# Kernel tuning notes

Hardware: AMD Instinct MI355X
Metric: run time of the kernel (lower is better)

## Reference

```python
import jax, jax.numpy as jnp
import numpy as np

N, E, B = 50000, 800000, 64
F_IN, HID, H, L = 128, 128, 4, 4
C = HID // H  # per-head channels = 32
NEG_SLOPE = 0.2  # PyG GATConv default leaky_relu slope


def setup_inputs() -> dict:
    key = jax.random.key(0)
    ks = iter(jax.random.split(key, 32))
    rn = lambda shape, s=0.05: jax.random.normal(next(ks), shape, jnp.float32) * s
    x = jax.random.normal(next(ks), (N, F_IN), jnp.float32)
    edge_index = jax.random.randint(next(ks), (2, E), 0, N, jnp.int32)
    edge_attr = jax.random.uniform(next(ks), (E, 2), dtype=jnp.float32)
    batch = jnp.sort(jax.random.randint(next(ks), (N,), 0, B, jnp.int32))
    return {
        "x": x, "edge_attr": edge_attr,
        "Win": rn((F_IN, HID)), "b_in": jnp.zeros((HID,), jnp.float32),
        "We1": rn((2, 16)), "be1": jnp.zeros((16,), jnp.float32),
        "We2": rn((16, H)), "be2": jnp.zeros((H,), jnp.float32),
        "Wl": rn((L, HID, HID)), "a_src": rn((L, H, C)), "a_dst": rn((L, H, C)),
        "bl": jnp.zeros((L, HID), jnp.float32),
        "ln_g": jnp.ones((L, HID), jnp.float32), "ln_b": jnp.zeros((L, HID), jnp.float32),
        "Wg1": rn((HID, HID // 2)), "bg1": jnp.zeros((HID // 2,), jnp.float32),
        "Wg2": rn((HID // 2, 1)), "bg2": jnp.zeros((1,), jnp.float32),
        "edge_index": edge_index, "batch": batch,
    }


def _layer_norm(x, g, b, eps=1e-5):
    mu = x.mean(-1, keepdims=True)
    var = ((x - mu) ** 2).mean(-1, keepdims=True)
    return (x - mu) * jax.lax.rsqrt(var + eps) * g + b


def _gat_conv(h, src, dst, W, a_s, a_d, bias):
    # PyG GATConv (shared lin for src/dst), add_self_loops already in src/dst.
    xp = (h @ W).reshape(N, H, C)            # [N,H,C]
    as_n = (xp * a_s).sum(-1)                # [N,H]
    ad_n = (xp * a_d).sum(-1)                # [N,H]
    e = jax.nn.leaky_relu(as_n[src] + ad_n[dst], NEG_SLOPE)   # [E+N,H]
    m = jax.ops.segment_max(e, dst, num_segments=N)           # stable softmax per dst
    p = jnp.exp(e - m[dst])
    s = jax.ops.segment_sum(p, dst, num_segments=N)
    alpha = p / (s[dst] + 1e-16)
    out = jax.ops.segment_sum(xp[src] * alpha[..., None], dst, num_segments=N)
    return out.reshape(N, HID) + bias


def reference(x, edge_attr, Win, b_in, We1, be1, We2, be2, Wl, a_src, a_dst, bl,
              ln_g, ln_b, Wg1, bg1, Wg2, bg2, edge_index, batch):
    h = x @ Win + b_in                                   # input_proj
    # edge bias MLP -> per-edge scalar -> scatter_add crit_signal (no self loops)
    edge_bias = jax.nn.relu(edge_attr @ We1 + be1) @ We2 + be2   # [E,H]
    edge_scalar = edge_bias.mean(axis=1)                         # [E]
    crit = jnp.zeros((N,), h.dtype).at[edge_index[1]].add(edge_scalar)[:, None]
    # self loops for GATConv
    loop = jnp.arange(N, dtype=edge_index.dtype)
    src = jnp.concatenate([edge_index[0], loop])
    dst = jnp.concatenate([edge_index[1], loop])
    for i in range(L):  # fixed small layer count
        h_new = _gat_conv(h, src, dst, Wl[i], a_src[i], a_dst[i], bl[i])
        h_new = _layer_norm(h_new, ln_g[i], ln_b[i])
        h_new = h_new + crit                             # broadcast [N,1]
        h = h_new + h                                    # residual (shapes match); dropout=eval noop
    # GlobalAttention pooling: softmax(gate) over each graph, weighted sum
    gate = jnp.tanh(h @ Wg1 + bg1) @ Wg2 + bg2           # [N,1]
    gmax = jax.ops.segment_max(gate, batch, num_segments=B)
    gp = jnp.exp(gate - gmax[batch])
    gs = jax.ops.segment_sum(gp, batch, num_segments=B)
    gate_sm = gp / (gs[batch] + 1e-16)
    return jax.ops.segment_sum(gate_sm * h, batch, num_segments=B)   # [B,HID]
```

## Files before the change

### kernel.cpp

```cpp
#include <hip/hip_runtime.h>
#include <math.h>

#define N_NODES 50000
#define N_EDGES 800000
#define N_B     64

typedef __attribute__((ext_vector_type(8))) short v8s;
typedef __attribute__((ext_vector_type(4))) float v4f;

__device__ __forceinline__ float lrelu(float x){ return x > 0.f ? x : 0.2f*x; }
__device__ __forceinline__ unsigned short f2b(float f){
  unsigned u = __float_as_uint(f);
  return (unsigned short)((u + 0x7fffu + ((u >> 16) & 1u)) >> 16);
}
__device__ __forceinline__ float blo(unsigned u){ return __uint_as_float(u << 16); }
__device__ __forceinline__ float bhi(unsigned u){ return __uint_as_float(u & 0xffff0000u); }

__global__ void k_conv(const float* __restrict__ x, const float* __restrict__ Win,
                       const float* __restrict__ Wl, const float* __restrict__ a_src,
                       const float* __restrict__ a_dst, const float* __restrict__ Wg1,
                       unsigned short* __restrict__ xb, unsigned short* __restrict__ WinT,
                       unsigned short* __restrict__ WlT, unsigned short* __restrict__ Wg1T){
  int i = blockIdx.x*256 + threadIdx.x;
  if (i < 1600000){
    float4 v = ((const float4*)x)[i];
    ushort4 p; p.x=f2b(v.x); p.y=f2b(v.y); p.z=f2b(v.z); p.w=f2b(v.w);
    ((ushort4*)xb)[i] = p;
    return;
  }
  i -= 1600000;
  if (i < 16384){
    int n = i >> 7, k = i & 127;
    WinT[n*128+k] = f2b(Win[k*128+n]);
    return;
  }
  i -= 16384;
  if (i < 65536){
    int l = i >> 14, n = (i >> 7) & 127, k = i & 127;
    WlT[l*144*128 + n*128 + k] = f2b(Wl[l*16384 + k*128 + n]);
    return;
  }
  i -= 65536;
  if (i < 4096){
    int l = i >> 10, k = (i >> 3) & 127, t = i & 7;
    int hh = t & 3, sd = t >> 2;
    const float* av = (sd ? a_dst : a_src) + l*128 + hh*32;
    const float* wr = Wl + l*16384 + k*128 + hh*32;
    float s = 0.f;
    #pragma unroll
    for (int c = 0; c < 32; c++) s = fmaf(wr[c], av[c], s);
    WlT[l*144*128 + (128 + sd*4 + hh)*128 + k] = f2b(s);
    return;
  }
  i -= 4096;
  if (i < 4096){
    int l = i >> 10, r = (i >> 7) & 7, k = i & 127;
    WlT[l*144*128 + (136+r)*128 + k] = 0;
    return;
  }
  i -= 4096;
  if (i < 8192){
    int n = i >> 7, k = i & 127;
    Wg1T[n*128+k] = f2b(Wg1[k*64+n]);
  }
}

__global__ void k_setup(const int* __restrict__ batch, int* __restrict__ start,
                        int* __restrict__ cnt){
  int i = blockIdx.x*256 + threadIdx.x;
  if (i >= N_NODES) return;
  cnt[i] = 0;
  int b = batch[i];
  int bp = (i == 0) ? -1 : batch[i-1];
  for (int j = bp+1; j <= b; j++) start[j] = i;
  if (i == N_NODES-1){
    for (int j = b+1; j <= N_B; j++) start[j] = N_NODES;
  }
}

__global__ void k_hist(const int* __restrict__ ei, int* __restrict__ cnt, int* __restrict__ rank){
  int t = blockIdx.x*256 + threadIdx.x;
  if (t >= 200000) return;
  #pragma unroll
  for (int r = 0; r < 4; r++){
    int e = t + r*200000;
    int d = ei[N_EDGES + e];
    rank[e] = atomicAdd(&cnt[d], 1);
  }
}

__global__ void k_scan1(const int* __restrict__ cnt, int* __restrict__ incl, int* __restrict__ part){
  __shared__ int sh[256];
  int tid = threadIdx.x, i = blockIdx.x*256 + tid;
  int v = (i < N_NODES) ? cnt[i] : 0;
  sh[tid] = v; __syncthreads();
  for (int off = 1; off < 256; off <<= 1){
    int t = (tid >= off) ? sh[tid-off] : 0;
    __syncthreads();
    sh[tid] += t; __syncthreads();
  }
  if (i < N_NODES) incl[i] = sh[tid];
  if (tid == 255) part[blockIdx.x] = sh[255];
}
__global__ void k_scan2(const int* __restrict__ part, int* __restrict__ pexcl, int nblocks){
  __shared__ int sh[256];
  int tid = threadIdx.x;
  int v = (tid < nblocks) ? part[tid] : 0;
  sh[tid] = v; __syncthreads();
  for (int off = 1; off < 256; off <<= 1){
    int t = (tid >= off) ? sh[tid-off] : 0;
    __syncthreads();
    sh[tid] += t; __syncthreads();
  }
  if (tid < nblocks) pexcl[tid] = sh[tid] - v;
}
__global__ void k_scan3(const int* __restrict__ cnt, const int* __restrict__ incl,
                        const int* __restrict__ pexcl, int* __restrict__ off){
  int i = blockIdx.x*256 + threadIdx.x;
  if (i >= N_NODES) return;
  int e = incl[i] - cnt[i] + pexcl[i >> 8];
  off[i] = e;
  if (i == N_NODES-1) off[N_NODES] = e + cnt[i];
}

__global__ void k_fill(const float* __restrict__ ea, const float* __restrict__ We1,
                       const float* __restrict__ be1, const float* __restrict__ We2,
                       const float* __restrict__ be2, const int* __restrict__ ei,
                       const int* __restrict__ off, const int* __restrict__ rank,
                       int2* __restrict__ es){
  __shared__ float w0[16], w1[16], bb[16], w2s[16];
  __shared__ float b2s;
  int tid = threadIdx.x;
  if (tid < 16){
    w0[tid] = We1[tid]; w1[tid] = We1[16+tid]; bb[tid] = be1[tid];
    w2s[tid] = 0.25f*(We2[tid*4]+We2[tid*4+1]+We2[tid*4+2]+We2[tid*4+3]);
  }
  if (tid == 0) b2s = 0.25f*(be2[0]+be2[1]+be2[2]+be2[3]);
  __syncthreads();
  int t = blockIdx.x*256 + tid;
  if (t >= 200000) return;
  #pragma unroll
  for (int r = 0; r < 4; r++){
    int e = t + r*200000;
    float a0 = ea[2*e], a1 = ea[2*e+1];
    float s = b2s;
    #pragma unroll
    for (int j = 0; j < 16; j++){
      float v = fmaf(a0, w0[j], fmaf(a1, w1[j], bb[j]));
      v = v > 0.f ? v : 0.f;
      s = fmaf(v, w2s[j], s);
    }
    int d = ei[N_EDGES + e];
    int p = off[d] + rank[e];
    es[p] = make_int2(ei[e], __float_as_int(s));
  }
}

template<int NT, int MODE>
__global__ __launch_bounds__(256) void k_mgemm(
    const unsigned short* __restrict__ A, const unsigned short* __restrict__ Bt,
    const float* __restrict__ bias,
    float* __restrict__ h, unsigned short* __restrict__ hb,
    unsigned short* __restrict__ xpb, float* __restrict__ asn, float* __restrict__ adn,
    const float* __restrict__ Wg2, const float* __restrict__ bg2, float* __restrict__ gate)
{
  __shared__ __attribute__((aligned(16))) unsigned short Bs[NT*16][136];
  __shared__ __attribute__((aligned(16))) unsigned short As[4][16][136];
  int tid = threadIdx.x, wave = tid >> 6, lane = tid & 63;
  int l15 = lane & 15, quad = lane >> 4;
  int rbase = blockIdx.x * 64;
  for (int id = tid; id < NT*16*16; id += 256){
    int r = id >> 4, ch = id & 15;
    *(v8s*)&Bs[r][ch*8] = *(const v8s*)(Bt + r*128 + ch*8);
  }
  for (int id = tid; id < 64*16; id += 256){
    int r = id >> 4, ch = id & 15;
    int gr = rbase + r;
    v8s v = {0,0,0,0,0,0,0,0};
    if (gr < N_NODES) v = *(const v8s*)(A + (size_t)gr*128 + ch*8);
    *(v8s*)&As[r >> 4][r & 15][ch*8] = v;
  }
  __syncthreads();
  v4f acc[NT];
  #pragma unroll
  for (int t = 0; t < NT; t++) acc[t] = (v4f){0.f,0.f,0.f,0.f};
  #pragma unroll
  for (int kb = 0; kb < 4; kb++){
    v8s a = *(v8s*)&As[wave][l15][kb*32 + quad*8];
    #pragma unroll
    for (int ct = 0; ct < NT; ct++){
      v8s b = *(v8s*)&Bs[ct*16 + l15][kb*32 + quad*8];
      acc[ct] = __builtin_amdgcn_mfma_f32_16x16x32_bf16(a, b, acc[ct], 0, 0, 0);
    }
  }
  int row0 = rbase + wave*16 + quad*4;
  if (MODE == 0){
    #pragma unroll
    for (int ct = 0; ct < 8; ct++){
      float bcol = bias[ct*16 + l15];
      #pragma unroll
      for (int r = 0; r < 4; r++){
        int gr = row0 + r;
        if (gr < N_NODES){
          float v = acc[ct][r] + bcol;
          h[(size_t)gr*128 + ct*16 + l15] = v;
          hb[(size_t)gr*128 + ct*16 + l15] = f2b(v);
        }
      }
    }
  } else if (MODE == 1){
    #pragma unroll
    for (int ct = 0; ct < 8; ct++){
      #pragma unroll
      for (int r = 0; r < 4; r++){
        int gr = row0 + r;
        if (gr < N_NODES) xpb[(size_t)gr*128 + ct*16 + l15] = f2b(acc[ct][r]);
      }
    }
    #pragma unroll
    for (int r = 0; r < 4; r++){
      int gr = row0 + r;
      if (gr < N_NODES){
        float v = acc[NT-1][r];
        if (l15 < 4) asn[gr*4 + l15] = v;
        else if (l15 < 8) adn[gr*4 + (l15-4)] = v;
      }
    }
  } else {
    float part[4] = {0.f,0.f,0.f,0.f};
    #pragma unroll
    for (int ct = 0; ct < NT; ct++){
      float b1 = bias[ct*16 + l15];
      float w2 = Wg2[ct*16 + l15];
      #pragma unroll
      for (int r = 0; r < 4; r++) part[r] = fmaf(tanhf(acc[ct][r] + b1), w2, part[r]);
    }
    #pragma unroll
    for (int m = 1; m < 16; m <<= 1){
      #pragma unroll
      for (int r = 0; r < 4; r++) part[r] += __shfl_xor(part[r], m);
    }
    if (l15 == 0){
      float b2 = bg2[0];
      #pragma unroll
      for (int r = 0; r < 4; r++){
        int gr = row0 + r;
        if (gr < N_NODES) gate[gr] = part[r] + b2;
      }
    }
  }
}

template<bool CRIT>
__global__ __launch_bounds__(256) void k_aggr(
    const unsigned short* __restrict__ xpb, const float* __restrict__ asn,
    const float* __restrict__ adn, const int* __restrict__ off,
    const int2* __restrict__ es,
    const float* __restrict__ bl, const float* __restrict__ lng,
    const float* __restrict__ lnb, float* __restrict__ crit,
    float* __restrict__ h, unsigned short* __restrict__ hb)
{
  __shared__ float lp[4][256];
  int wave = threadIdx.x >> 6, lane = threadIdx.x & 63;
  int n = blockIdx.x*4 + wave;
  if (n >= N_NODES) return;
  int base = off[n], deg = off[n+1] - base;
  float4 ad4 = *(const float4*)(adn + n*4);
  float4 asf = *(const float4*)(asn + n*4);
  float ex = lrelu(asf.x+ad4.x), ey = lrelu(asf.y+ad4.y);
  float ez = lrelu(asf.z+ad4.z), ew = lrelu(asf.w+ad4.w);
  const unsigned* xw = (const unsigned*)xpb;
  float* myp = &lp[wave][0];
  int hh = lane >> 4;
  float acc0, acc1, sx, sy, sz, sw, cr;
  float psx, psy, psz, psw;

  if (deg <= 64){
    int sreg = 0;
    float e0 = -3.0e38f, e1 = -3.0e38f, e2 = -3.0e38f, e3 = -3.0e38f;
    float cw = 0.f;
    if (lane < deg){
      int2 er = es[base + lane];
      sreg = er.x;
      float4 a = *(const float4*)(asn + sreg*4);
      e0 = lrelu(a.x+ad4.x); e1 = lrelu(a.y+ad4.y);
      e2 = lrelu(a.z+ad4.z); e3 = lrelu(a.w+ad4.w);
      if (CRIT) cw = __int_as_float(er.y);
    }
    float mx = fmaxf(e0,ex), my = fmaxf(e1,ey), mz = fmaxf(e2,ez), mw = fmaxf(e3,ew);
    #pragma unroll
    for (int m = 1; m < 64; m <<= 1){
      mx = fmaxf(mx, __shfl_xor(mx, m)); my = fmaxf(my, __shfl_xor(my, m));
      mz = fmaxf(mz, __shfl_xor(mz, m)); mw = fmaxf(mw, __shfl_xor(mw, m));
      if (CRIT) cw += __shfl_xor(cw, m);
    }
    if (CRIT){ if (lane == 0) crit[n] = cw; cr = cw; }
    else cr = crit[n];
    psx = __expf(ex-mx); psy = __expf(ey-my); psz = __expf(ez-mz); psw = __expf(ew-mw);
    float p0 = 0.f, p1 = 0.f, p2 = 0.f, p3 = 0.f;
    if (lane < deg){
      p0 = __expf(e0-mx); p1 = __expf(e1-my); p2 = __expf(e2-mz); p3 = __expf(e3-mw);
    }
    sx = p0; sy = p1; sz = p2; sw = p3;
    *(float4*)(&myp[4*lane]) = make_float4(p0,p1,p2,p3);
    __threadfence_block();
    float pself = hh < 2 ? (hh == 0 ? psx : psy) : (hh == 2 ? psz : psw);
    unsigned us = (xw + ((size_t)(unsigned)n << 6))[lane];
    acc0 = pself * blo(us); acc1 = pself * bhi(us);
    int degR = (deg + 7) & ~7;
    for (int c = 0; c < degR; c += 8){
      unsigned u[8];
      #pragma unroll
      for (int k = 0; k < 8; k++){
        int s0 = __builtin_amdgcn_readlane(sreg, c + k);
        u[k] = (xw + ((size_t)(unsigned)s0 << 6))[lane];
      }
      #pragma unroll
      for (int k = 0; k < 8; k++){
        float q = myp[4*(c+k) + hh];
        acc0 = fmaf(q, blo(u[k]), acc0);
        acc1 = fmaf(q, bhi(u[k]), acc1);
      }
    }
    __threadfence_block();
  } else {
    float mx = ex, my = ey, mz = ez, mw = ew;
    float cw = 0.f;
    for (int j = lane; j < deg; j += 64){
      int2 er = es[base + j];
      float4 a = *(const float4*)(asn + er.x*4);
      mx = fmaxf(mx, lrelu(a.x+ad4.x)); my = fmaxf(my, lrelu(a.y+ad4.y));
      mz = fmaxf(mz, lrelu(a.z+ad4.z)); mw = fmaxf(mw, lrelu(a.w+ad4.w));
      if (CRIT) cw += __int_as_float(er.y);
    }
    #pragma unroll
    for (int m = 1; m < 64; m <<= 1){
      mx = fmaxf(mx, __shfl_xor(mx, m)); my = fmaxf(my, __shfl_xor(my, m));
      mz = fmaxf(mz, __shfl_xor(mz, m)); mw = fmaxf(mw, __shfl_xor(mw, m));
      if (CRIT) cw += __shfl_xor(cw, m);
    }
    if (CRIT){ if (lane == 0) crit[n] = cw; cr = cw; }
    else cr = crit[n];
    psx = __expf(ex-mx); psy = __expf(ey-my); psz = __expf(ez-mz); psw = __expf(ew-mw);
    float pself = hh < 2 ? (hh == 0 ? psx : psy) : (hh == 2 ? psz : psw);
    unsigned us = (xw + ((size_t)(unsigned)n << 6))[lane];
    acc0 = pself * blo(us); acc1 = pself * bhi(us);
    sx = 0.f; sy = 0.f; sz = 0.f; sw = 0.f;
    for (int j0 = 0; j0 < deg; j0 += 64){
      int clen = deg - j0; if (clen > 64) clen = 64;
      int sreg = 0;
      float p0 = 0.f, p1 = 0.f, p2 = 0.f, p3 = 0.f;
      if (lane < clen){
        sreg = es[base + j0 + lane].x;
        float4 a = *(const float4*)(asn + sreg*4);
        p0 = __expf(lrelu(a.x+ad4.x)-mx);
        p1 = __expf(lrelu(a.y+ad4.y)-my);
        p2 = __expf(lrelu(a.z+ad4.z)-mz);
        p3 = __expf(lrelu(a.w+ad4.w)-mw);
        sx += p0; sy += p1; sz += p2; sw += p3;
      }
      *(float4*)(&myp[4*lane]) = make_float4(p0,p1,p2,p3);
      __threadfence_block();
      int clenR = (clen + 7) & ~7;
      for (int c = 0; c < clenR; c += 8){
        unsigned u[8];
        #pragma unroll
        for (int k = 0; k < 8; k++){
          int s0 = __builtin_amdgcn_readlane(sreg, c + k);
          u[k] = (xw + ((size_t)(unsigned)s0 << 6))[lane];
        }
        #pragma unroll
        for (int k = 0; k < 8; k++){
          float q = myp[4*(c+k) + hh];
          acc0 = fmaf(q, blo(u[k]), acc0);
          acc1 = fmaf(q, bhi(u[k]), acc1);
        }
      }
      __threadfence_block();
    }
  }
  #pragma unroll
  for (int m = 1; m < 64; m <<= 1){
    sx += __shfl_xor(sx, m); sy += __shfl_xor(sy, m);
    sz += __shfl_xor(sz, m); sw += __shfl_xor(sw, m);
  }
  sx += psx; sy += psy; sz += psz; sw += psw;
  float den = (hh < 2 ? (hh == 0 ? sx : sy) : (hh == 2 ? sz : sw)) + 1e-16f;
  float rden = 1.f / den;
  int c0 = 2*lane;
  float2 blv = *(const float2*)(bl + c0);
  float o0 = acc0*rden + blv.x;
  float o1 = acc1*rden + blv.y;
  float su = o0 + o1, sq = o0*o0 + o1*o1;
  #pragma unroll
  for (int m = 1; m < 64; m <<= 1){ su += __shfl_xor(su, m); sq += __shfl_xor(sq, m); }
  float mu  = su * (1.f/128.f);
  float var = sq * (1.f/128.f) - mu*mu; var = var > 0.f ? var : 0.f;
  float inv = rsqrtf(var + 1e-5f);
  float2 rv  = *(const float2*)(h + (size_t)n*128 + c0);
  float2 gv  = *(const float2*)(lng + c0);
  float2 bv2 = *(const float2*)(lnb + c0);
  o0 = (o0-mu)*inv*gv.x + bv2.x + cr + rv.x;
  o1 = (o1-mu)*inv*gv.y + bv2.y + cr + rv.y;
  *(float2*)(&h[(size_t)n*128 + c0]) = make_float2(o0, o1);
  *(unsigned*)(&hb[(size_t)n*128 + c0]) = ((unsigned)f2b(o1) << 16) | f2b(o0);
}

__global__ __launch_bounds__(256) void k_pool(
    const float* __restrict__ h, float* __restrict__ gate,
    const int* __restrict__ start, float* __restrict__ out)
{
  __shared__ float red[4];
  __shared__ float sbc;
  __shared__ float4 accs[8][32];
  int b = blockIdx.x;
  int s0 = start[b], s1 = start[b+1];
  int tid = threadIdx.x, lane = tid & 63, wave = tid >> 6;
  float m = -3.0e38f;
  for (int i = s0 + tid; i < s1; i += 256) m = fmaxf(m, gate[i]);
  #pragma unroll
  for (int k = 1; k < 64; k <<= 1) m = fmaxf(m, __shfl_xor(m, k));
  if (lane == 0) red[wave] = m;
  __syncthreads();
  if (tid == 0) sbc = fmaxf(fmaxf(red[0],red[1]), fmaxf(red[2],red[3]));
  __syncthreads();
  float gm = sbc;
  __syncthreads();
  float s = 0.f;
  for (int i = s0 + tid; i < s1; i += 256){
    float p = __expf(gate[i] - gm);
    gate[i] = p;
    s += p;
  }
  #pragma unroll
  for (int k = 1; k < 64; k <<= 1) s += __shfl_xor(s, k);
  if (lane == 0) red[wave] = s;
  __syncthreads();
  if (tid == 0) sbc = red[0]+red[1]+red[2]+red[3];
  __syncthreads();
  float inv = 1.f / (sbc + 1e-16f);
  int c4 = (tid & 31) * 4;
  int g  = tid >> 5;
  float4 acc = make_float4(0.f,0.f,0.f,0.f);
  for (int i = s0 + g; i < s1; i += 8){
    float p = gate[i];
    float4 hv = *(const float4*)(h + (size_t)i*128 + c4);
    acc.x = fmaf(p,hv.x,acc.x); acc.y = fmaf(p,hv.y,acc.y);
    acc.z = fmaf(p,hv.z,acc.z); acc.w = fmaf(p,hv.w,acc.w);
  }
  accs[g][tid & 31] = acc;
  __syncthreads();
  if (g == 0){
    float4 t = acc;
    #pragma unroll
    for (int k = 1; k < 8; k++){
      float4 o = accs[k][tid & 31];
      t.x += o.x; t.y += o.y; t.z += o.z; t.w += o.w;
    }
    t.x *= inv; t.y *= inv; t.z *= inv; t.w *= inv;
    *(float4*)(out + b*128 + c4) = t;
  }
}

extern "C" void kernel_launch(void* const* d_in, const int* in_sizes, int n_in,
                              void* d_out, int out_size, void* d_ws, size_t ws_size,
                              hipStream_t stream){
  (void)in_sizes; (void)n_in; (void)out_size; (void)ws_size;
  const float* x    = (const float*)d_in[0];
  const float* ea   = (const float*)d_in[1];
  const float* Win  = (const float*)d_in[2];
  const float* b_in = (const float*)d_in[3];
  const float* We1  = (const float*)d_in[4];
  const float* be1  = (const float*)d_in[5];
  const float* We2  = (const float*)d_in[6];
  const float* be2  = (const float*)d_in[7];
  const float* Wl   = (const float*)d_in[8];
  const float* a_src= (const float*)d_in[9];
  const float* a_dst= (const float*)d_in[10];
  const float* bl   = (const float*)d_in[11];
  const float* lng  = (const float*)d_in[12];
  const float* lnb  = (const float*)d_in[13];
  const float* Wg1  = (const float*)d_in[14];
  const float* bg1  = (const float*)d_in[15];
  const float* Wg2  = (const float*)d_in[16];
  const float* bg2  = (const float*)d_in[17];
  const int*   ei   = (const int*)d_in[18];
  const int*   batch= (const int*)d_in[19];
  float* out = (float*)d_out;

  char* w = (char*)d_ws;
  auto alloc = [&](size_t bytes){ char* p = w; w += (bytes + 255) & ~(size_t)255; return p; };
  float* h    = (float*)alloc((size_t)N_NODES*128*4);
  unsigned short* hb  = (unsigned short*)alloc((size_t)N_NODES*128*2);
  unsigned short* xpb = (unsigned short*)alloc((size_t)N_NODES*128*2);
  float* asn  = (float*)alloc((size_t)N_NODES*4*4);
  float* adn  = (float*)alloc((size_t)N_NODES*4*4);
  float* crit = (float*)alloc((size_t)N_NODES*4);
  int*   cnt  = (int*)alloc((size_t)N_NODES*4);
  int*   incl = (int*)alloc((size_t)N_NODES*4);
  int*   part = (int*)alloc(256*4);
  int*   pexc = (int*)alloc(256*4);
  int*   off  = (int*)alloc((size_t)(N_NODES+1)*4);
  int*   rank = (int*)alloc((size_t)N_EDGES*4);
  int2*  es   = (int2*)alloc((size_t)N_EDGES*8);
  float* gate = (float*)alloc((size_t)N_NODES*4);
  int*   start= (int*)alloc((size_t)(N_B+1)*4);
  unsigned short* WinT = (unsigned short*)alloc((size_t)128*128*2);
  unsigned short* WlT  = (unsigned short*)alloc((size_t)4*144*128*2);
  unsigned short* Wg1T = (unsigned short*)alloc((size_t)64*128*2);
  unsigned short* xb = xpb;

  int nb_n = (N_NODES + 255)/256;
  int nb_w = (N_NODES + 3)/4;
  int nb_g = (N_NODES + 63)/64;
  int nb_c = (1698304 + 255)/256;
  int nb_4e = (200000 + 255)/256;

  k_conv<<<nb_c,256,0,stream>>>(x, Win, Wl, a_src, a_dst, Wg1, xb, WinT, WlT, Wg1T);
  k_setup<<<nb_n,256,0,stream>>>(batch, start, cnt);
  k_hist<<<nb_4e,256,0,stream>>>(ei, cnt, rank);
  k_mgemm<8,0><<<nb_g,256,0,stream>>>(xb, WinT, b_in, h, hb,
                                      nullptr, nullptr, nullptr, nullptr, nullptr, nullptr);
  k_scan1<<<nb_n,256,0,stream>>>(cnt, incl, part);
  k_scan2<<<1,256,0,stream>>>(part, pexc, nb_n);
  k_scan3<<<nb_n,256,0,stream>>>(cnt, incl, pexc, off);
  k_fill<<<nb_4e,256,0,stream>>>(ea, We1, be1, We2, be2, ei, off, rank, es);
  for (int l = 0; l < 4; l++){
    k_mgemm<9,1><<<nb_g,256,0,stream>>>(hb, WlT + (size_t)l*144*128, nullptr, nullptr, nullptr,
                                        xpb, asn, adn, nullptr, nullptr, nullptr);
    if (l == 0)
      k_aggr<true><<<nb_w,256,0,stream>>>(xpb, asn, adn, off, es,
                                          bl + l*128, lng + l*128, lnb + l*128, crit, h, hb);
    else
      k_aggr<false><<<nb_w,256,0,stream>>>(xpb, asn, adn, off, es,
                                           bl + l*128, lng + l*128, lnb + l*128, crit, h, hb);
  }
  k_mgemm<4,2><<<nb_g,256,0,stream>>>(hb, Wg1T, bg1, nullptr, nullptr,
                                      nullptr, nullptr, nullptr, Wg2, bg2, gate);
  k_pool<<<N_B,256,0,stream>>>(h, gate, start, out);
}
```

Baseline: 482.4 us.

## Process two nodes per wave in aggregation; fuse x conversion and scans

The aggregation kernel now gives each wavefront two destination nodes and interleaves their gather loads and FMAs, so more independent memory requests are in flight per wave. Nodes with degree above 64 fall back to a shared general path. The separate fp32-to-bf16 pass over x is folded into the first GEMM's tile load, and the second and third scan kernels are merged, which removes two launches and one full pass over x. The cost is higher register pressure, and the paired loop runs to the larger of the two degrees, wasting work when the degrees differ.

```diff
diff --git a/kernel.cpp b/kernel.cpp
--- a/kernel.cpp
+++ b/kernel.cpp
@@ -7,6 +7,7 @@
 
 typedef __attribute__((ext_vector_type(8))) short v8s;
 typedef __attribute__((ext_vector_type(4))) float v4f;
+typedef __attribute__((ext_vector_type(2))) float v2f;
 
 __device__ __forceinline__ float lrelu(float x){ return x > 0.f ? x : 0.2f*x; }
 __device__ __forceinline__ unsigned short f2b(float f){
@@ -16,19 +17,12 @@
 __device__ __forceinline__ float blo(unsigned u){ return __uint_as_float(u << 16); }
 __device__ __forceinline__ float bhi(unsigned u){ return __uint_as_float(u & 0xffff0000u); }
 
-__global__ void k_conv(const float* __restrict__ x, const float* __restrict__ Win,
-                       const float* __restrict__ Wl, const float* __restrict__ a_src,
-                       const float* __restrict__ a_dst, const float* __restrict__ Wg1,
-                       unsigned short* __restrict__ xb, unsigned short* __restrict__ WinT,
-                       unsigned short* __restrict__ WlT, unsigned short* __restrict__ Wg1T){
+__global__ void k_conv(const float* __restrict__ Win, const float* __restrict__ Wl,
+                       const float* __restrict__ a_src, const float* __restrict__ a_dst,
+                       const float* __restrict__ Wg1,
+                       unsigned short* __restrict__ WinT, unsigned short* __restrict__ WlT,
+                       unsigned short* __restrict__ Wg1T){
   int i = blockIdx.x*256 + threadIdx.x;
-  if (i < 1600000){
-    float4 v = ((const float4*)x)[i];
-    ushort4 p; p.x=f2b(v.x); p.y=f2b(v.y); p.z=f2b(v.z); p.w=f2b(v.w);
-    ((ushort4*)xb)[i] = p;
-    return;
-  }
-  i -= 1600000;
   if (i < 16384){
     int n = i >> 7, k = i & 127;
     WinT[n*128+k] = f2b(Win[k*128+n]);
@@ -102,23 +96,21 @@
   if (i < N_NODES) incl[i] = sh[tid];
   if (tid == 255) part[blockIdx.x] = sh[255];
 }
-__global__ void k_scan2(const int* __restrict__ part, int* __restrict__ pexcl, int nblocks){
-  __shared__ int sh[256];
-  int tid = threadIdx.x;
-  int v = (tid < nblocks) ? part[tid] : 0;
-  sh[tid] = v; __syncthreads();
-  for (int off = 1; off < 256; off <<= 1){
-    int t = (tid >= off) ? sh[tid-off] : 0;
-    __syncthreads();
-    sh[tid] += t; __syncthreads();
-  }
-  if (tid < nblocks) pexcl[tid] = sh[tid] - v;
-}
-__global__ void k_scan3(const int* __restrict__ cnt, const int* __restrict__ incl,
-                        const int* __restrict__ pexcl, int* __restrict__ off){
-  int i = blockIdx.x*256 + threadIdx.x;
+__global__ void k_scan23(const int* __restrict__ cnt, const int* __restrict__ incl,
+                         const int* __restrict__ part, int* __restrict__ off){
+  __shared__ int red[4];
+  __shared__ int bsum;
+  int tid = threadIdx.x, lane = tid & 63, wave = tid >> 6;
+  int v = (tid < (int)blockIdx.x) ? part[tid] : 0;
+  #pragma unroll
+  for (int m = 1; m < 64; m <<= 1) v += __shfl_xor(v, m);
+  if (lane == 0) red[wave] = v;
+  __syncthreads();
+  if (tid == 0) bsum = red[0]+red[1]+red[2]+red[3];
+  __syncthreads();
+  int i = blockIdx.x*256 + tid;
   if (i >= N_NODES) return;
-  int e = incl[i] - cnt[i] + pexcl[i >> 8];
+  int e = incl[i] - cnt[i] + bsum;
   off[i] = e;
   if (i == N_NODES-1) off[N_NODES] = e + cnt[i];
 }
@@ -156,9 +148,9 @@
   }
 }
 
-template<int NT, int MODE>
+template<int NT, int MODE, bool AF32>
 __global__ __launch_bounds__(256) void k_mgemm(
-    const unsigned short* __restrict__ A, const unsigned short* __restrict__ Bt,
+    const void* __restrict__ A, const unsigned short* __restrict__ Bt,
     const float* __restrict__ bias,
     float* __restrict__ h, unsigned short* __restrict__ hb,
     unsigned short* __restrict__ xpb, float* __restrict__ asn, float* __restrict__ adn,
@@ -177,7 +169,17 @@
     int r = id >> 4, ch = id & 15;
     int gr = rbase + r;
     v8s v = {0,0,0,0,0,0,0,0};
-    if (gr < N_NODES) v = *(const v8s*)(A + (size_t)gr*128 + ch*8);
+    if (gr < N_NODES){
+      if (AF32){
+        const float* Af = (const float*)A + (size_t)gr*128 + ch*8;
+        float4 va = *(const float4*)Af;
+        float4 vb = *(const float4*)(Af + 4);
+        v[0]=(short)f2b(va.x); v[1]=(short)f2b(va.y); v[2]=(short)f2b(va.z); v[3]=(short)f2b(va.w);
+        v[4]=(short)f2b(vb.x); v[5]=(short)f2b(vb.y); v[6]=(short)f2b(vb.z); v[7]=(short)f2b(vb.w);
+      } else {
+        v = *(const v8s*)((const unsigned short*)A + (size_t)gr*128 + ch*8);
+      }
+    }
     *(v8s*)&As[r >> 4][r & 15][ch*8] = v;
   }
   __syncthreads();
@@ -252,63 +254,57 @@
 }
 
 template<bool CRIT>
-__global__ __launch_bounds__(256) void k_aggr(
-    const unsigned short* __restrict__ xpb, const float* __restrict__ asn,
-    const float* __restrict__ adn, const int* __restrict__ off,
-    const int2* __restrict__ es,
-    const float* __restrict__ bl, const float* __restrict__ lng,
-    const float* __restrict__ lnb, float* __restrict__ crit,
-    float* __restrict__ h, unsigned short* __restrict__ hb)
+__device__ void aggr_node_general(int n, int base, int deg, int lane, float* myp,
+    const unsigned* xw, const float* __restrict__ asn, const float* __restrict__ adn,
+    const int2* __restrict__ es, const float* __restrict__ bl,
+    const float* __restrict__ lng, const float* __restrict__ lnb,
+    float* __restrict__ crit, float* __restrict__ h, unsigned short* __restrict__ hb)
 {
-  __shared__ float lp[4][256];
-  int wave = threadIdx.x >> 6, lane = threadIdx.x & 63;
-  int n = blockIdx.x*4 + wave;
-  if (n >= N_NODES) return;
-  int base = off[n], deg = off[n+1] - base;
   float4 ad4 = *(const float4*)(adn + n*4);
   float4 asf = *(const float4*)(asn + n*4);
   float ex = lrelu(asf.x+ad4.x), ey = lrelu(asf.y+ad4.y);
   float ez = lrelu(asf.z+ad4.z), ew = lrelu(asf.w+ad4.w);
-  const unsigned* xw = (const unsigned*)xpb;
-  float* myp = &lp[wave][0];
   int hh = lane >> 4;
-  float acc0, acc1, sx, sy, sz, sw, cr;
-  float psx, psy, psz, psw;
-
-  if (deg <= 64){
+  float mx = ex, my = ey, mz = ez, mw = ew;
+  float cw = 0.f;
+  for (int j = lane; j < deg; j += 64){
+    int2 er = es[base + j];
+    float4 a = *(const float4*)(asn + er.x*4);
+    mx = fmaxf(mx, lrelu(a.x+ad4.x)); my = fmaxf(my, lrelu(a.y+ad4.y));
+    mz = fmaxf(mz, lrelu(a.z+ad4.z)); mw = fmaxf(mw, lrelu(a.w+ad4.w));
+    if (CRIT) cw += __int_as_float(er.y);
+  }
+  #pragma unroll
+  for (int m = 1; m < 64; m <<= 1){
+    mx = fmaxf(mx, __shfl_xor(mx, m)); my = fmaxf(my, __shfl_xor(my, m));
+    mz = fmaxf(mz, __shfl_xor(mz, m)); mw = fmaxf(mw, __shfl_xor(mw, m));
+    if (CRIT) cw += __shfl_xor(cw, m);
+  }
+  float cr;
+  if (CRIT){ if (lane == 0) crit[n] = cw; cr = cw; }
+  else cr = crit[n];
+  float psx = __expf(ex-mx), psy = __expf(ey-my), psz = __expf(ez-mz), psw = __expf(ew-mw);
+  float pself = hh < 2 ? (hh == 0 ? psx : psy) : (hh == 2 ? psz : psw);
+  unsigned us = (xw + ((size_t)(unsigned)n << 6))[lane];
+  float acc0 = pself * blo(us), acc1 = pself * bhi(us);
+  float sx = 0.f, sy = 0.f, sz = 0.f, sw = 0.f;
+  for (int j0 = 0; j0 < deg; j0 += 64){
+    int clen = deg - j0; if (clen > 64) clen = 64;
     int sreg = 0;
-    float e0 = -3.0e38f, e1 = -3.0e38f, e2 = -3.0e38f, e3 = -3.0e38f;
-    float cw = 0.f;
-    if (lane < deg){
-      int2 er = es[base + lane];
-      sreg = er.x;
+    float p0 = 0.f, p1 = 0.f, p2 = 0.f, p3 = 0.f;
+    if (lane < clen){
+      sreg = es[base + j0 + lane].x;
       float4 a = *(const float4*)(asn + sreg*4);
-      e0 = lrelu(a.x+ad4.x); e1 = lrelu(a.y+ad4.y);
-      e2 = lrelu(a.z+ad4.z); e3 = lrelu(a.w+ad4.w);
-      if (CRIT) cw = __int_as_float(er.y);
-    }
-    float mx = fmaxf(e0,ex), my = fmaxf(e1,ey), mz = fmaxf(e2,ez), mw = fmaxf(e3,ew);
-    #pragma unroll
-    for (int m = 1; m < 64; m <<= 1){
-      mx = fmaxf(mx, __shfl_xor(mx, m)); my = fmaxf(my, __shfl_xor(my, m));
-      mz = fmaxf(mz, __shfl_xor(mz, m)); mw = fmaxf(mw, __shfl_xor(mw, m));
-      if (CRIT) cw += __shfl_xor(cw, m);
-    }
-    if (CRIT){ if (lane == 0) crit[n] = cw; cr = cw; }
-    else cr = crit[n];
-    psx = __expf(ex-mx); psy = __expf(ey-my); psz = __expf(ez-mz); psw = __expf(ew-mw);
-    float p0 = 0.f, p1 = 0.f, p2 = 0.f, p3 = 0.f;
-    if (lane < deg){
-      p0 = __expf(e0-mx); p1 = __expf(e1-my); p2 = __expf(e2-mz); p3 = __expf(e3-mw);
-    }
-    sx = p0; sy = p1; sz = p2; sw = p3;
+      p0 = __expf(lrelu(a.x+ad4.x)-mx);
+      p1 = __expf(lrelu(a.y+ad4.y)-my);
+      p2 = __expf(lrelu(a.z+ad4.z)-mz);
+      p3 = __expf(lrelu(a.w+ad4.w)-mw);
+      sx += p0; sy += p1; sz += p2; sw += p3;
+    }
     *(float4*)(&myp[4*lane]) = make_float4(p0,p1,p2,p3);
     __threadfence_block();
-    float pself = hh < 2 ? (hh == 0 ? psx : psy) : (hh == 2 ? psz : psw);
-    unsigned us = (xw + ((size_t)(unsigned)n << 6))[lane];
-    acc0 = pself * blo(us); acc1 = pself * bhi(us);
-    int degR = (deg + 7) & ~7;
-    for (int c = 0; c < degR; c += 8){
+    int clenR = (clen + 7) & ~7;
+    for (int c = 0; c < clenR; c += 8){
       unsigned u[8];
       #pragma unroll
       for (int k = 0; k < 8; k++){
@@ -323,61 +319,6 @@
       }
     }
     __threadfence_block();
-  } else {
-    float mx = ex, my = ey, mz = ez, mw = ew;
-    float cw = 0.f;
-    for (int j = lane; j < deg; j += 64){
-      int2 er = es[base + j];
-      float4 a = *(const float4*)(asn + er.x*4);
-      mx = fmaxf(mx, lrelu(a.x+ad4.x)); my = fmaxf(my, lrelu(a.y+ad4.y));
-      mz = fmaxf(mz, lrelu(a.z+ad4.z)); mw = fmaxf(mw, lrelu(a.w+ad4.w));
-      if (CRIT) cw += __int_as_float(er.y);
-    }
-    #pragma unroll
-    for (int m = 1; m < 64; m <<= 1){
-      mx = fmaxf(mx, __shfl_xor(mx, m)); my = fmaxf(my, __shfl_xor(my, m));
-      mz = fmaxf(mz, __shfl_xor(mz, m)); mw = fmaxf(mw, __shfl_xor(mw, m));
-      if (CRIT) cw += __shfl_xor(cw, m);
-    }
-    if (CRIT){ if (lane == 0) crit[n] = cw; cr = cw; }
-    else cr = crit[n];
-    psx = __expf(ex-mx); psy = __expf(ey-my); psz = __expf(ez-mz); psw = __expf(ew-mw);
-    float pself = hh < 2 ? (hh == 0 ? psx : psy) : (hh == 2 ? psz : psw);
-    unsigned us = (xw + ((size_t)(unsigned)n << 6))[lane];
-    acc0 = pself * blo(us); acc1 = pself * bhi(us);
-    sx = 0.f; sy = 0.f; sz = 0.f; sw = 0.f;
-    for (int j0 = 0; j0 < deg; j0 += 64){
-      int clen = deg - j0; if (clen > 64) clen = 64;
-      int sreg = 0;
-      float p0 = 0.f, p1 = 0.f, p2 = 0.f, p3 = 0.f;
-      if (lane < clen){
-        sreg = es[base + j0 + lane].x;
-        float4 a = *(const float4*)(asn + sreg*4);
-        p0 = __expf(lrelu(a.x+ad4.x)-mx);
-        p1 = __expf(lrelu(a.y+ad4.y)-my);
-        p2 = __expf(lrelu(a.z+ad4.z)-mz);
-        p3 = __expf(lrelu(a.w+ad4.w)-mw);
-        sx += p0; sy += p1; sz += p2; sw += p3;
-      }
-      *(float4*)(&myp[4*lane]) = make_float4(p0,p1,p2,p3);
-      __threadfence_block();
-      int clenR = (clen + 7) & ~7;
-      for (int c = 0; c < clenR; c += 8){
-        unsigned u[8];
-        #pragma unroll
-        for (int k = 0; k < 8; k++){
-          int s0 = __builtin_amdgcn_readlane(sreg, c + k);
-          u[k] = (xw + ((size_t)(unsigned)s0 << 6))[lane];
-        }
-        #pragma unroll
-        for (int k = 0; k < 8; k++){
-          float q = myp[4*(c+k) + hh];
-          acc0 = fmaf(q, blo(u[k]), acc0);
-          acc1 = fmaf(q, bhi(u[k]), acc1);
-        }
-      }
-      __threadfence_block();
-    }
   }
   #pragma unroll
   for (int m = 1; m < 64; m <<= 1){
@@ -404,6 +345,160 @@
   o1 = (o1-mu)*inv*gv.y + bv2.y + cr + rv.y;
   *(float2*)(&h[(size_t)n*128 + c0]) = make_float2(o0, o1);
   *(unsigned*)(&hb[(size_t)n*128 + c0]) = ((unsigned)f2b(o1) << 16) | f2b(o0);
+}
+
+template<bool CRIT>
+__global__ __launch_bounds__(256) void k_aggr(
+    const unsigned short* __restrict__ xpb, const float* __restrict__ asn,
+    const float* __restrict__ adn, const int* __restrict__ off,
+    const int2* __restrict__ es,
+    const float* __restrict__ bl, const float* __restrict__ lng,
+    const float* __restrict__ lnb, float* __restrict__ crit,
+    float* __restrict__ h, unsigned short* __restrict__ hb)
+{
+  __shared__ float lp[4][2][256];
+  int wave = threadIdx.x >> 6, lane = threadIdx.x & 63;
+  int n0 = blockIdx.x*8 + wave*2;
+  int n1 = n0 + 1;
+  int b0 = off[n0], b1 = off[n1], b2 = off[n1+1];
+  int deg0 = b1 - b0, deg1 = b2 - b1;
+  const unsigned* xw = (const unsigned*)xpb;
+  if (deg0 > 64 || deg1 > 64){
+    aggr_node_general<CRIT>(n0, b0, deg0, lane, &lp[wave][0][0], xw, asn, adn, es,
+                            bl, lng, lnb, crit, h, hb);
+    aggr_node_general<CRIT>(n1, b1, deg1, lane, &lp[wave][1][0], xw, asn, adn, es,
+                            bl, lng, lnb, crit, h, hb);
+    return;
+  }
+  float4 ad0 = *(const float4*)(adn + n0*4);
+  float4 as0 = *(const float4*)(asn + n0*4);
+  float4 ad1 = *(const float4*)(adn + n1*4);
+  float4 as1 = *(const float4*)(asn + n1*4);
+  float ex0 = lrelu(as0.x+ad0.x), ey0 = lrelu(as0.y+ad0.y);
+  float ez0 = lrelu(as0.z+ad0.z), ew0 = lrelu(as0.w+ad0.w);
+  float ex1 = lrelu(as1.x+ad1.x), ey1 = lrelu(as1.y+ad1.y);
+  float ez1 = lrelu(as1.z+ad1.z), ew1 = lrelu(as1.w+ad1.w);
+  int sreg0 = 0, sreg1 = 0;
+  float c0w = 0.f, c1w = 0.f;
+  float e00=-3.0e38f, e01=-3.0e38f, e02=-3.0e38f, e03=-3.0e38f;
+  float e10=-3.0e38f, e11=-3.0e38f, e12=-3.0e38f, e13=-3.0e38f;
+  if (lane < deg0){
+    int2 er = es[b0 + lane];
+    sreg0 = er.x;
+    float4 a = *(const float4*)(asn + sreg0*4);
+    e00 = lrelu(a.x+ad0.x); e01 = lrelu(a.y+ad0.y);
+    e02 = lrelu(a.z+ad0.z); e03 = lrelu(a.w+ad0.w);
+    if (CRIT) c0w = __int_as_float(er.y);
+  }
+  if (lane < deg1){
+    int2 er = es[b1 + lane];
+    sreg1 = er.x;
+    float4 a = *(const float4*)(asn + sreg1*4);
+    e10 = lrelu(a.x+ad1.x); e11 = lrelu(a.y+ad1.y);
+    e12 = lrelu(a.z+ad1.z); e13 = lrelu(a.w+ad1.w);
+    if (CRIT) c1w = __int_as_float(er.y);
+  }
+  float mx0 = fmaxf(e00,ex0), my0 = fmaxf(e01,ey0), mz0 = fmaxf(e02,ez0), mw0 = fmaxf(e03,ew0);
+  float mx1 = fmaxf(e10,ex1), my1 = fmaxf(e11,ey1), mz1 = fmaxf(e12,ez1), mw1 = fmaxf(e13,ew1);
+  #pragma unroll
+  for (int m = 1; m < 64; m <<= 1){
+    mx0 = fmaxf(mx0, __shfl_xor(mx0, m)); my0 = fmaxf(my0, __shfl_xor(my0, m));
+    mz0 = fmaxf(mz0, __shfl_xor(mz0, m)); mw0 = fmaxf(mw0, __shfl_xor(mw0, m));
+    mx1 = fmaxf(mx1, __shfl_xor(mx1, m)); my1 = fmaxf(my1, __shfl_xor(my1, m));
+    mz1 = fmaxf(mz1, __shfl_xor(mz1, m)); mw1 = fmaxf(mw1, __shfl_xor(mw1, m));
+    if (CRIT){ c0w += __shfl_xor(c0w, m); c1w += __shfl_xor(c1w, m); }
+  }
+  float cr0, cr1;
+  if (CRIT){
+    if (lane == 0){ crit[n0] = c0w; crit[n1] = c1w; }
+    cr0 = c0w; cr1 = c1w;
+  } else { cr0 = crit[n0]; cr1 = crit[n1]; }
+  float ps0x = __expf(ex0-mx0), ps0y = __expf(ey0-my0), ps0z = __expf(ez0-mz0), ps0w = __expf(ew0-mw0);
+  float ps1x = __expf(ex1-mx1), ps1y = __expf(ey1-my1), ps1z = __expf(ez1-mz1), ps1w = __expf(ew1-mw1);
+  float p00=0.f,p01=0.f,p02=0.f,p03=0.f, p10=0.f,p11=0.f,p12=0.f,p13=0.f;
+  if (lane < deg0){
+    p00 = __expf(e00-mx0); p01 = __expf(e01-my0); p02 = __expf(e02-mz0); p03 = __expf(e03-mw0);
+  }
+  if (lane < deg1){
+    p10 = __expf(e10-mx1); p11 = __expf(e11-my1); p12 = __expf(e12-mz1); p13 = __expf(e13-mw1);
+  }
+  float s0x=p00, s0y=p01, s0z=p02, s0w=p03;
+  float s1x=p10, s1y=p11, s1z=p12, s1w=p13;
+  float* myp0 = &lp[wave][0][0];
+  float* myp1 = &lp[wave][1][0];
+  *(float4*)(&myp0[4*lane]) = make_float4(p00,p01,p02,p03);
+  *(float4*)(&myp1[4*lane]) = make_float4(p10,p11,p12,p13);
+  __threadfence_block();
+  int hh = lane >> 4;
+  float pself0 = hh < 2 ? (hh == 0 ? ps0x : ps0y) : (hh == 2 ? ps0z : ps0w);
+  float pself1 = hh < 2 ? (hh == 0 ? ps1x : ps1y) : (hh == 2 ? ps1z : ps1w);
+  unsigned us0 = (xw + ((size_t)(unsigned)n0 << 6))[lane];
+  unsigned us1 = (xw + ((size_t)(unsigned)n1 << 6))[lane];
+  v2f acc0 = {pself0*blo(us0), pself0*bhi(us0)};
+  v2f acc1 = {pself1*blo(us1), pself1*bhi(us1)};
+  int dmax = deg0 > deg1 ? deg0 : deg1;
+  int degR = (dmax + 7) & ~7;
+  for (int c = 0; c < degR; c += 8){
+    unsigned u0[8], u1[8];
+    #pragma unroll
+    for (int k = 0; k < 8; k++){
+      int s = __builtin_amdgcn_readlane(sreg0, c + k);
+      u0[k] = (xw + ((size_t)(unsigned)s << 6))[lane];
+    }
+    #pragma unroll
+    for (int k = 0; k < 8; k++){
+      int s = __builtin_amdgcn_readlane(sreg1, c + k);
+      u1[k] = (xw + ((size_t)(unsigned)s << 6))[lane];
+    }
+    #pragma unroll
+    for (int k = 0; k < 8; k++){
+      float q0 = myp0[4*(c+k) + hh];
+      float q1 = myp1[4*(c+k) + hh];
+      v2f v0 = {blo(u0[k]), bhi(u0[k])};
+      v2f v1 = {blo(u1[k]), bhi(u1[k])};
+      acc0 += q0 * v0;
+      acc1 += q1 * v1;
+    }
+  }
+  #pragma unroll
+  for (int m = 1; m < 64; m <<= 1){
+    s0x += __shfl_xor(s0x, m); s0y += __shfl_xor(s0y, m);
+    s0z += __shfl_xor(s0z, m); s0w += __shfl_xor(s0w, m);
+    s1x += __shfl_xor(s1x, m); s1y += __shfl_xor(s1y, m);
+    s1z += __shfl_xor(s1z, m); s1w += __shfl_xor(s1w, m);
+  }
+  s0x += ps0x; s0y += ps0y; s0z += ps0z; s0w += ps0w;
+  s1x += ps1x; s1y += ps1y; s1z += ps1z; s1w += ps1w;
+  float den0 = (hh < 2 ? (hh == 0 ? s0x : s0y) : (hh == 2 ? s0z : s0w)) + 1e-16f;
+  float den1 = (hh < 2 ? (hh == 0 ? s1x : s1y) : (hh == 2 ? s1z : s1w)) + 1e-16f;
+  float rden0 = 1.f / den0, rden1 = 1.f / den1;
+  int ch = 2*lane;
+  float2 blv = *(const float2*)(bl + ch);
+  float o00 = acc0.x*rden0 + blv.x, o01 = acc0.y*rden0 + blv.y;
+  float o10 = acc1.x*rden1 + blv.x, o11 = acc1.y*rden1 + blv.y;
+  float su0 = o00 + o01, sq0 = o00*o00 + o01*o01;
+  float su1 = o10 + o11, sq1 = o10*o10 + o11*o11;
+  #pragma unroll
+  for (int m = 1; m < 64; m <<= 1){
+    su0 += __shfl_xor(su0, m); sq0 += __shfl_xor(sq0, m);
+    su1 += __shfl_xor(su1, m); sq1 += __shfl_xor(sq1, m);
+  }
+  float mu0 = su0*(1.f/128.f), mu1 = su1*(1.f/128.f);
+  float var0 = sq0*(1.f/128.f) - mu0*mu0; var0 = var0 > 0.f ? var0 : 0.f;
+  float var1 = sq1*(1.f/128.f) - mu1*mu1; var1 = var1 > 0.f ? var1 : 0.f;
+  float inv0 = rsqrtf(var0 + 1e-5f), inv1 = rsqrtf(var1 + 1e-5f);
+  float2 gv  = *(const float2*)(lng + ch);
+  float2 bv2 = *(const float2*)(lnb + ch);
+  float2 rv0 = *(const float2*)(h + (size_t)n0*128 + ch);
+  float2 rv1 = *(const float2*)(h + (size_t)n1*128 + ch);
+  o00 = (o00-mu0)*inv0*gv.x + bv2.x + cr0 + rv0.x;
+  o01 = (o01-mu0)*inv0*gv.y + bv2.y + cr0 + rv0.y;
+  o10 = (o10-mu1)*inv1*gv.x + bv2.x + cr1 + rv1.x;
+  o11 = (o11-mu1)*inv1*gv.y + bv2.y + cr1 + rv1.y;
+  *(float2*)(&h[(size_t)n0*128 + ch]) = make_float2(o00, o01);
+  *(float2*)(&h[(size_t)n1*128 + ch]) = make_float2(o10, o11);
+  *(unsigned*)(&hb[(size_t)n0*128 + ch]) = ((unsigned)f2b(o01) << 16) | f2b(o00);
+  *(unsigned*)(&hb[(size_t)n1*128 + ch]) = ((unsigned)f2b(o11) << 16) | f2b(o10);
 }
 
 __global__ __launch_bounds__(256) void k_pool(
@@ -499,7 +594,6 @@
   int*   cnt  = (int*)alloc((size_t)N_NODES*4);
   int*   incl = (int*)alloc((size_t)N_NODES*4);
   int*   part = (int*)alloc(256*4);
-  int*   pexc = (int*)alloc(256*4);
   int*   off  = (int*)alloc((size_t)(N_NODES+1)*4);
   int*   rank = (int*)alloc((size_t)N_EDGES*4);
   int2*  es   = (int2*)alloc((size_t)N_EDGES*8);
@@ -508,34 +602,33 @@
   unsigned short* WinT = (unsigned short*)alloc((size_t)128*128*2);
   unsigned short* WlT  = (unsigned short*)alloc((size_t)4*144*128*2);
   unsigned short* Wg1T = (unsigned short*)alloc((size_t)64*128*2);
-  unsigned short* xb = xpb;
 
   int nb_n = (N_NODES + 255)/256;
-  int nb_w = (N_NODES + 3)/4;
+  int nb_a = 6250;
   int nb_g = (N_NODES + 63)/64;
-  int nb_c = (1698304 + 255)/256;
+  int nb_c = (98304 + 255)/256;
   int nb_4e = (200000 + 255)/256;
 
-  k_conv<<<nb_c,256,0,stream>>>(x, Win, Wl, a_src, a_dst, Wg1, xb, WinT, WlT, Wg1T);
+  k_conv<<<nb_c,256,0,stream>>>(Win, Wl, a_src, a_dst, Wg1, WinT, WlT, Wg1T);
   k_setup<<<nb_n,256,0,stream>>>(batch, start, cnt);
   k_hist<<<nb_4e,256,0,stream>>>(ei, cnt, rank);
-  k_mgemm<8,0><<<nb_g,256,0,stream>>>(xb, WinT, b_in, h, hb,
-                                      nullptr, nullptr, nullptr, nullptr, nullptr, nullptr);
+  k_mgemm<8,0,true><<<nb_g,256,0,stream>>>((const void*)x, WinT, b_in, h, hb,
+                                           nullptr, nullptr, nullptr, nullptr, nullptr, nullptr);
   k_scan1<<<nb_n,256,0,stream>>>(cnt, incl, part);
-  k_scan2<<<1,256,0,stream>>>(part, pexc, nb_n);
-  k_scan3<<<nb_n,256,0,stream>>>(cnt, incl, pexc, off);
+  k_scan23<<<nb_n,256,0,stream>>>(cnt, incl, part, off);
   k_fill<<<nb_4e,256,0,stream>>>(ea, We1, be1, We2, be2, ei, off, rank, es);
   for (int l = 0; l < 4; l++){
-    k_mgemm<9,1><<<nb_g,256,0,stream>>>(hb, WlT + (size_t)l*144*128, nullptr, nullptr, nullptr,
-                                        xpb, asn, adn, nullptr, nullptr, nullptr);
+    k_mgemm<9,1,false><<<nb_g,256,0,stream>>>((const void*)hb, WlT + (size_t)l*144*128, nullptr,
+                                              nullptr, nullptr, xpb, asn, adn,
+                                              nullptr, nullptr, nullptr);
     if (l == 0)
-      k_aggr<true><<<nb_w,256,0,stream>>>(xpb, asn, adn, off, es,
+      k_aggr<true><<<nb_a,256,0,stream>>>(xpb, asn, adn, off, es,
                                           bl + l*128, lng + l*128, lnb + l*128, crit, h, hb);
     else
-      k_aggr<false><<<nb_w,256,0,stream>>>(xpb, asn, adn, off, es,
+      k_aggr<false><<<nb_a,256,0,stream>>>(xpb, asn, adn, off, es,
                                            bl + l*128, lng + l*128, lnb + l*128, crit, h, hb);
   }
-  k_mgemm<4,2><<<nb_g,256,0,stream>>>(hb, Wg1T, bg1, nullptr, nullptr,
-                                      nullptr, nullptr, nullptr, Wg2, bg2, gate);
+  k_mgemm<4,2,false><<<nb_g,256,0,stream>>>((const void*)hb, Wg1T, bg1, nullptr, nullptr,
+                                            nullptr, nullptr, nullptr, Wg2, bg2, gate);
   k_pool<<<N_B,256,0,stream>>>(h, gate, start, out);
 }
```

Result: no change. 490.9 us (+1.8%).
